# Optimization experiments

Measured on AMD Instinct MI355X. Metric: run time of the kernel, lower is better.

## Reference

```python
import jax, jax.numpy as jnp
import numpy as np

B, SQ, SK, D, DV = 16, 2048, 2048, 64, 64
DROPOUT_P = 0.1


def setup_inputs() -> dict:
    key = jax.random.key(0)
    k1, k2, k3, k4 = jax.random.split(key, 4)
    return {
        "query": jax.random.normal(k1, (B, SQ, D), dtype=jnp.float32),
        "key": jax.random.normal(k2, (B, SK, D), dtype=jnp.float32),
        "value": jax.random.normal(k3, (B, SK, DV), dtype=jnp.float32),
        "drop_mask": jax.random.uniform(k4, (B, SQ, SK), dtype=jnp.float32),
    }


def reference(query, key, value, drop_mask):
    # scaled dot-product attention with explicit score matrix, as in the module
    scale = jnp.sqrt(jnp.asarray(key.shape[-1], dtype=query.dtype))
    qk = jnp.einsum("bqd,bkd->bqk", query, key) / scale  # [B, SQ, SK]
    attn = jax.nn.softmax(qk, axis=-1)
    # dropout: keep where uniform > p, rescale by 1/(1-p)
    keep = (drop_mask > DROPOUT_P).astype(attn.dtype)
    attn = attn * keep / (1.0 - DROPOUT_P)
    return jnp.einsum("bqk,bkv->bqv", attn, value)  # [B, SQ, DV]
```

## Files before the change

### kernel.cpp

```cpp
#include <hip/hip_runtime.h>
#include <hip/hip_bf16.h>

#define B_ 16
#define SQ_ 2048
#define SK_ 2048
#define D_ 64
#define DV_ 64
#define INV_KEEP 1.1111111f

typedef float f4 __attribute__((ext_vector_type(4)));
typedef __bf16 bf16x2 __attribute__((ext_vector_type(2)));
typedef __bf16 bf16x8 __attribute__((ext_vector_type(8)));
typedef short s16x4 __attribute__((ext_vector_type(4)));
typedef unsigned int u32;
typedef unsigned int u32x2 __attribute__((ext_vector_type(2)));
typedef unsigned int u32x4 __attribute__((ext_vector_type(4)));

static __device__ __forceinline__ unsigned short bf16u(float f) {
    u32 u = __builtin_bit_cast(u32, f);
    u += 0x7fffu + ((u >> 16) & 1u);
    return (unsigned short)(u >> 16);
}
static __device__ __forceinline__ u32 pk2(float lo, float hi) {
    return (u32)bf16u(lo) | ((u32)bf16u(hi) << 16);
}
static __device__ __forceinline__ u32 pkc(float lo, float hi) {
    bf16x2 t = {(__bf16)lo, (__bf16)hi};
    return __builtin_bit_cast(u32, t);
}

static __device__ __forceinline__ void gload16(const void* g, void* l) {
    __builtin_amdgcn_global_load_lds(
        (const __attribute__((address_space(1))) unsigned int*)g,
        (__attribute__((address_space(3))) unsigned int*)l, 16, 0, 0);
}

static __device__ __forceinline__ f4 mfma16(s16x4 a, s16x4 b, f4 c) {
#if __has_builtin(__builtin_amdgcn_mfma_f32_16x16x16bf16_1k)
    return __builtin_amdgcn_mfma_f32_16x16x16bf16_1k(a, b, c, 0, 0, 0);
#else
    f4 d;
    asm("v_mfma_f32_16x16x16_bf16 %0, %1, %2, %3" : "=v"(d) : "v"(a), "v"(b), "v"(c));
    return d;
#endif
}

__global__ __launch_bounds__(256) void k_retile(const float* __restrict__ K,
                                                unsigned short* __restrict__ KbT) {
    int b = blockIdx.x >> 6, kt = blockIdx.x & 63;
    int t = threadIdx.x;
    int row = t >> 3, dc = t & 7;
    const float* src = K + ((size_t)(b * SK_ + kt * 32 + row)) * D_ + dc * 8;
    f4 a = *(const f4*)src;
    f4 b2 = *(const f4*)(src + 4);
    u32x4 w;
    w[0] = pk2(a.x, a.y); w[1] = pk2(a.z, a.w);
    w[2] = pk2(b2.x, b2.y); w[3] = pk2(b2.z, b2.w);
    *(u32x4*)(KbT + ((size_t)(b * 64 + kt)) * 2048 + (dc * 32 + row) * 8) = w;
}

__global__ __launch_bounds__(256) void v_retile(const float* __restrict__ V,
                                                unsigned short* __restrict__ VtT) {
    __shared__ float vt[32][65];
    int b = blockIdx.x >> 6, kt = blockIdx.x & 63;
    int t = threadIdx.x;
#pragma unroll
    for (int e = 0; e < 2; ++e) {
        int f = t * 2 + e;
        int row = f >> 4, c4 = (f & 15) * 4;
        *(f4*)&vt[row][c4] = *(const f4*)(V + ((size_t)(b * SK_ + kt * 32 + row)) * DV_ + c4);
    }
    __syncthreads();
    unsigned short* dst = VtT + ((size_t)(b * 64 + kt)) * 2048 + (size_t)t * 8;
    u32x4 w;
#pragma unroll
    for (int e = 0; e < 2; ++e) {
        int s = t * 2 + e;
        int kq = s >> 6, v = s & 63;
        w[e * 2 + 0] = pk2(vt[kq * 4 + 0][v], vt[kq * 4 + 1][v]);
        w[e * 2 + 1] = pk2(vt[kq * 4 + 2][v], vt[kq * 4 + 3][v]);
    }
    *(u32x4*)dst = w;
}

__global__ __launch_bounds__(256) void compress_mask(const float* __restrict__ mask,
                                                     u32* __restrict__ bits) {
    int strip = blockIdx.x;
    int b  = strip >> 7;
    int q0 = (strip & 127) << 4;
    int w    = threadIdx.x >> 6;
    int lane = threadIdx.x & 63;
    int g = lane >> 4, c = lane & 15;
    const float* mrow = mask + ((size_t)(b * SQ_ + q0 + c)) * SK_ + 4 * g;
    u32x4 outw;
#pragma unroll
    for (int tgl = 0; tgl < 4; ++tgl) {
        int tg = w * 4 + tgl;
        u32 word = 0;
#pragma unroll
        for (int ti = 0; ti < 4; ++ti) {
            const float* p = mrow + tg * 128 + ti * 32;
            f4 lo = *(const f4*)(p);
            f4 hi = *(const f4*)(p + 16);
            u32 by = 0;
#pragma unroll
            for (int r = 0; r < 4; ++r) {
                by |= (lo[r] > 0.1f ? (1u << r) : 0u);
                by |= (hi[r] > 0.1f ? (1u << (4 + r)) : 0u);
            }
            word |= by << (8 * ti);
        }
        outw[tgl] = word;
    }
    *(u32x4*)(bits + ((size_t)strip * 64 + lane) * 16 + w * 4) = outw;
}

template <int SPLIT>
__global__ __launch_bounds__(256) void attn_main(const float* __restrict__ Q,
                                                 const unsigned short* __restrict__ KbT,
                                                 const unsigned short* __restrict__ VtT,
                                                 const u32* __restrict__ bits,
                                                 float* __restrict__ out,
                                                 float* __restrict__ accP,
                                                 float* __restrict__ lP) {
    constexpr int NT32 = SK_ / SPLIT / 32;
    constexpr int NB = 512 * SPLIT;
    constexpr int NWORDS = NT32 / 4;
    __shared__ unsigned short sK[2][2048];
    __shared__ unsigned short sV[2][2048];

    int bswz = (blockIdx.x & 7) * (NB / 8) + (blockIdx.x >> 3);
    int wid  = threadIdx.x >> 6;
    int split = bswz & (SPLIT - 1);
    int strip = (bswz / SPLIT) * 4 + wid;
    int b  = strip >> 7;
    int q0 = (strip & 127) << 4;
    int lane = threadIdx.x & 63;
    int g = lane >> 4, c = lane & 15;

    const size_t tile0 = ((size_t)b * 64 + split * NT32) * 2048;
    const unsigned short* ksrc = KbT + tile0 + (size_t)threadIdx.x * 8;
    const unsigned short* vsrc = VtT + tile0 + (size_t)threadIdx.x * 8;

    gload16(ksrc, &sK[0][wid * 512]);
    gload16(vsrc, &sV[0][wid * 512]);

    u32 bwAll[NWORDS];
    {
        const u32* bbase = bits + ((size_t)strip * 64 + lane) * 16 + split * NWORDS;
#pragma unroll
        for (int n = 0; n < NWORDS / 4; ++n)
            *(u32x4*)&bwAll[n * 4] = *(const u32x4*)(bbase + n * 4);
    }

    bf16x8 qf[2];
    {
        const float* qp = Q + ((size_t)(b * SQ_ + q0 + c)) * D_ + 8 * g;
#pragma unroll
        for (int h = 0; h < 2; ++h) {
            f4 a  = *(const f4*)(qp + h * 32);
            f4 bq = *(const f4*)(qp + h * 32 + 4);
            u32x4 wq;
            wq[0] = pk2(a.x * 0.125f, a.y * 0.125f);
            wq[1] = pk2(a.z * 0.125f, a.w * 0.125f);
            wq[2] = pk2(bq.x * 0.125f, bq.y * 0.125f);
            wq[3] = pk2(bq.z * 0.125f, bq.w * 0.125f);
            qf[h] = __builtin_bit_cast(bf16x8, wq);
        }
    }

    const unsigned short* kbL = &sK[0][0] + g * 256 + c * 8;
    const unsigned short* vbL = &sV[0][0] + g * 256 + c * 4;

    f4 acc[4];
#pragma unroll
    for (int vb = 0; vb < 4; ++vb) acc[vb] = (f4){0.f, 0.f, 0.f, 0.f};
    float lsum[2][4];
#pragma unroll
    for (int t = 0; t < 2; ++t)
#pragma unroll
        for (int r = 0; r < 4; ++r) lsum[t][r] = 0.f;

#pragma unroll
    for (int kt = 0; kt < NT32; ++kt) {
        const int cur = kt & 1;
        if (kt + 1 < NT32) {
            gload16(ksrc + (size_t)(kt + 1) * 2048, &sK[cur ^ 1][wid * 512]);
            gload16(vsrc + (size_t)(kt + 1) * 2048, &sV[cur ^ 1][wid * 512]);
            asm volatile("s_waitcnt vmcnt(2)" ::: "memory");
        } else {
            asm volatile("s_waitcnt vmcnt(0)" ::: "memory");
        }
        __builtin_amdgcn_s_barrier();
        asm volatile("" ::: "memory");

        const unsigned short* kB = kbL + cur * 2048;
        const unsigned short* vB = vbL + cur * 2048;
        const u32 mby = (bwAll[kt >> 2] >> ((kt & 3) * 8)) & 0xFFu;

        f4 st[2];
#pragma unroll
        for (int t = 0; t < 2; ++t) {
            u32x4 k0 = *(const u32x4*)(kB + t * 128);
            u32x4 k1 = *(const u32x4*)(kB + 1024 + t * 128);
            st[t] = (f4){0.f, 0.f, 0.f, 0.f};
            st[t] = __builtin_amdgcn_mfma_f32_16x16x32_bf16(
                __builtin_bit_cast(bf16x8, k0), qf[0], st[t], 0, 0, 0);
            st[t] = __builtin_amdgcn_mfma_f32_16x16x32_bf16(
                __builtin_bit_cast(bf16x8, k1), qf[1], st[t], 0, 0, 0);
        }
        float pd[2][4];
#pragma unroll
        for (int t = 0; t < 2; ++t)
#pragma unroll
            for (int r = 0; r < 4; ++r) {
                float p = __expf(st[t][r]);
                lsum[t][r] += p;
                pd[t][r] = (mby & (1u << (4 * t + r))) ? p : 0.f;
            }
#pragma unroll
        for (int t = 0; t < 2; ++t) {
            u32x2 pw;
            pw[0] = pkc(pd[t][0], pd[t][1]);
            pw[1] = pkc(pd[t][2], pd[t][3]);
            s16x4 pb = __builtin_bit_cast(s16x4, pw);
#pragma unroll
            for (int vb = 0; vb < 4; ++vb) {
                u32x2 vv = *(const u32x2*)(vB + t * 1024 + vb * 64);
                acc[vb] = mfma16(__builtin_bit_cast(s16x4, vv), pb, acc[vb]);
            }
        }

        asm volatile("" ::: "memory");
        __builtin_amdgcn_s_barrier();
        asm volatile("" ::: "memory");
    }

    float lf = 0.f;
#pragma unroll
    for (int t = 0; t < 2; ++t)
#pragma unroll
        for (int r = 0; r < 4; ++r) lf += lsum[t][r];
    lf += __shfl_xor(lf, 16);
    lf += __shfl_xor(lf, 32);

    if constexpr (SPLIT == 1) {
        float li = INV_KEEP / lf;
        float* op = out + ((size_t)(b * SQ_ + q0 + c)) * DV_;
#pragma unroll
        for (int vb = 0; vb < 4; ++vb) {
            f4 o = acc[vb] * li;
            __builtin_nontemporal_store(o, (f4*)(op + 16 * vb + 4 * g));
        }
    } else {
        float* ap = accP + (((size_t)strip * SPLIT + split) * 64 + lane) * 16;
#pragma unroll
        for (int vb = 0; vb < 4; ++vb)
            *(f4*)(ap + 4 * vb) = acc[vb];
        if (g == 0)
            lP[((size_t)strip * SPLIT + split) * 16 + c] = lf;
    }
}

__global__ __launch_bounds__(256) void attn_combine(const float* __restrict__ accP,
                                                    const float* __restrict__ lP,
                                                    float* __restrict__ out) {
    __shared__ float sacc[4 * 1280];
    __shared__ float sl[64];
    int strip = blockIdx.x;
    int t = threadIdx.x;
    const float* src = accP + (size_t)strip * 4096;
#pragma unroll
    for (int s = 0; s < 4; ++s)
        *(f4*)&sacc[s * 1280 + (t >> 2) * 20 + (t & 3) * 4] = *(const f4*)(src + s * 1024 + t * 4);
    if (t < 64) sl[t] = lP[(size_t)strip * 64 + t];
    __syncthreads();

    int q = t >> 4, j = t & 15;
    float L = sl[q] + sl[16 + q] + sl[32 + q] + sl[48 + q];
    float inv = INV_KEEP / L;
    int base = (16 * (j & 3) + q) * 20 + 4 * (j >> 2);
    f4 o = (f4){0.f, 0.f, 0.f, 0.f};
#pragma unroll
    for (int s = 0; s < 4; ++s)
        o += *(const f4*)&sacc[s * 1280 + base];
    o *= inv;
    int b  = strip >> 7;
    int q0 = (strip & 127) << 4;
    __builtin_nontemporal_store(o, (f4*)(out + ((size_t)(b * SQ_ + q0 + q)) * DV_ + 4 * j));
}

extern "C" void kernel_launch(void* const* d_in, const int* in_sizes, int n_in,
                              void* d_out, int out_size, void* d_ws, size_t ws_size,
                              hipStream_t stream) {
    const float* Q = (const float*)d_in[0];
    const float* K = (const float*)d_in[1];
    const float* V = (const float*)d_in[2];
    const float* M = (const float*)d_in[3];
    float* out = (float*)d_out;

    char* ws = (char*)d_ws;
    unsigned short* KbT  = (unsigned short*)ws;
    unsigned short* VtT  = (unsigned short*)(ws + (size_t)4  * 1024 * 1024);
    u32*            bits = (u32*)           (ws + (size_t)8  * 1024 * 1024);
    float*          accP = (float*)         (ws + (size_t)16 * 1024 * 1024);
    float*          lP   = (float*)         (ws + (size_t)48 * 1024 * 1024);

    const size_t need_split = (size_t)48 * 1024 * 1024 + (size_t)2048 * 64 * 4;

    k_retile<<<1024, 256, 0, stream>>>(K, KbT);
    v_retile<<<1024, 256, 0, stream>>>(V, VtT);
    compress_mask<<<2048, 256, 0, stream>>>(M, bits);
    if (ws_size >= need_split) {
        attn_main<4><<<2048, 256, 0, stream>>>(Q, KbT, VtT, bits, out, accP, lP);
        attn_combine<<<2048, 256, 0, stream>>>(accP, lP, out);
    } else {
        attn_main<1><<<512, 256, 0, stream>>>(Q, KbT, VtT, bits, out, nullptr, nullptr);
    }
}
```

Measured before the change: 108.9 us.

## Fuse dropout mask read into attention kernel via LDS double-buffering

Removes the separate compress_mask kernel and instead streams the float dropout mask directly into shared memory alongside the K and V tiles in the main attention loop, thresholding it in place. This avoids one kernel launch and the write-then-read of the packed bit mask in workspace. In exchange, the main kernel adds 16 KB of LDS per block for a float mask double-buffer and issues more async loads per iteration, which may reduce occupancy and lengthen the memory wait in the pipelined loop.

```diff
diff --git a/kernel.cpp b/kernel.cpp
--- a/kernel.cpp
+++ b/kernel.cpp
@@ -83,51 +83,19 @@
     *(u32x4*)dst = w;
 }
 
-__global__ __launch_bounds__(256) void compress_mask(const float* __restrict__ mask,
-                                                     u32* __restrict__ bits) {
-    int strip = blockIdx.x;
-    int b  = strip >> 7;
-    int q0 = (strip & 127) << 4;
-    int w    = threadIdx.x >> 6;
-    int lane = threadIdx.x & 63;
-    int g = lane >> 4, c = lane & 15;
-    const float* mrow = mask + ((size_t)(b * SQ_ + q0 + c)) * SK_ + 4 * g;
-    u32x4 outw;
-#pragma unroll
-    for (int tgl = 0; tgl < 4; ++tgl) {
-        int tg = w * 4 + tgl;
-        u32 word = 0;
-#pragma unroll
-        for (int ti = 0; ti < 4; ++ti) {
-            const float* p = mrow + tg * 128 + ti * 32;
-            f4 lo = *(const f4*)(p);
-            f4 hi = *(const f4*)(p + 16);
-            u32 by = 0;
-#pragma unroll
-            for (int r = 0; r < 4; ++r) {
-                by |= (lo[r] > 0.1f ? (1u << r) : 0u);
-                by |= (hi[r] > 0.1f ? (1u << (4 + r)) : 0u);
-            }
-            word |= by << (8 * ti);
-        }
-        outw[tgl] = word;
-    }
-    *(u32x4*)(bits + ((size_t)strip * 64 + lane) * 16 + w * 4) = outw;
-}
-
 template <int SPLIT>
 __global__ __launch_bounds__(256) void attn_main(const float* __restrict__ Q,
                                                  const unsigned short* __restrict__ KbT,
                                                  const unsigned short* __restrict__ VtT,
-                                                 const u32* __restrict__ bits,
+                                                 const float* __restrict__ mask,
                                                  float* __restrict__ out,
                                                  float* __restrict__ accP,
                                                  float* __restrict__ lP) {
     constexpr int NT32 = SK_ / SPLIT / 32;
     constexpr int NB = 512 * SPLIT;
-    constexpr int NWORDS = NT32 / 4;
     __shared__ unsigned short sK[2][2048];
     __shared__ unsigned short sV[2][2048];
+    __shared__ float sM[2][2048];
 
     int bswz = (blockIdx.x & 7) * (NB / 8) + (blockIdx.x >> 3);
     int wid  = threadIdx.x >> 6;
@@ -135,23 +103,19 @@
     int strip = (bswz / SPLIT) * 4 + wid;
     int b  = strip >> 7;
     int q0 = (strip & 127) << 4;
+    int kb = split * (SK_ / SPLIT);
     int lane = threadIdx.x & 63;
     int g = lane >> 4, c = lane & 15;
 
     const size_t tile0 = ((size_t)b * 64 + split * NT32) * 2048;
     const unsigned short* ksrc = KbT + tile0 + (size_t)threadIdx.x * 8;
     const unsigned short* vsrc = VtT + tile0 + (size_t)threadIdx.x * 8;
+    const float* msrc = mask + ((size_t)(b * SQ_ + q0 + (lane & 15))) * SK_ + kb + (lane >> 4) * 4;
 
     gload16(ksrc, &sK[0][wid * 512]);
     gload16(vsrc, &sV[0][wid * 512]);
-
-    u32 bwAll[NWORDS];
-    {
-        const u32* bbase = bits + ((size_t)strip * 64 + lane) * 16 + split * NWORDS;
-#pragma unroll
-        for (int n = 0; n < NWORDS / 4; ++n)
-            *(u32x4*)&bwAll[n * 4] = *(const u32x4*)(bbase + n * 4);
-    }
+    gload16(msrc,      &sM[0][wid * 512]);
+    gload16(msrc + 16, &sM[0][wid * 512 + 256]);
 
     bf16x8 qf[2];
     {
@@ -171,6 +135,7 @@
 
     const unsigned short* kbL = &sK[0][0] + g * 256 + c * 8;
     const unsigned short* vbL = &sV[0][0] + g * 256 + c * 4;
+    const float* mbL = &sM[0][0] + wid * 512 + (g * 16 + c) * 4;
 
     f4 acc[4];
 #pragma unroll
@@ -187,7 +152,9 @@
         if (kt + 1 < NT32) {
             gload16(ksrc + (size_t)(kt + 1) * 2048, &sK[cur ^ 1][wid * 512]);
             gload16(vsrc + (size_t)(kt + 1) * 2048, &sV[cur ^ 1][wid * 512]);
-            asm volatile("s_waitcnt vmcnt(2)" ::: "memory");
+            gload16(msrc + (kt + 1) * 32,      &sM[cur ^ 1][wid * 512]);
+            gload16(msrc + (kt + 1) * 32 + 16, &sM[cur ^ 1][wid * 512 + 256]);
+            asm volatile("s_waitcnt vmcnt(4)" ::: "memory");
         } else {
             asm volatile("s_waitcnt vmcnt(0)" ::: "memory");
         }
@@ -196,7 +163,9 @@
 
         const unsigned short* kB = kbL + cur * 2048;
         const unsigned short* vB = vbL + cur * 2048;
-        const u32 mby = (bwAll[kt >> 2] >> ((kt & 3) * 8)) & 0xFFu;
+        const float* mB = mbL + cur * 2048;
+        f4 mk0 = *(const f4*)(mB);
+        f4 mk1 = *(const f4*)(mB + 256);
 
         f4 st[2];
 #pragma unroll
@@ -211,13 +180,15 @@
         }
         float pd[2][4];
 #pragma unroll
-        for (int t = 0; t < 2; ++t)
+        for (int t = 0; t < 2; ++t) {
+            const f4 mk = t ? mk1 : mk0;
 #pragma unroll
             for (int r = 0; r < 4; ++r) {
                 float p = __expf(st[t][r]);
                 lsum[t][r] += p;
-                pd[t][r] = (mby & (1u << (4 * t + r))) ? p : 0.f;
+                pd[t][r] = (mk[r] > 0.1f) ? p : 0.f;
             }
+        }
 #pragma unroll
         for (int t = 0; t < 2; ++t) {
             u32x2 pw;
@@ -301,20 +272,18 @@
 
     char* ws = (char*)d_ws;
     unsigned short* KbT  = (unsigned short*)ws;
-    unsigned short* VtT  = (unsigned short*)(ws + (size_t)4  * 1024 * 1024);
-    u32*            bits = (u32*)           (ws + (size_t)8  * 1024 * 1024);
-    float*          accP = (float*)         (ws + (size_t)16 * 1024 * 1024);
-    float*          lP   = (float*)         (ws + (size_t)48 * 1024 * 1024);
-
-    const size_t need_split = (size_t)48 * 1024 * 1024 + (size_t)2048 * 64 * 4;
+    unsigned short* VtT  = (unsigned short*)(ws + (size_t)4 * 1024 * 1024);
+    float*          accP = (float*)         (ws + (size_t)8 * 1024 * 1024);
+    float*          lP   = (float*)         (ws + (size_t)40 * 1024 * 1024);
+
+    const size_t need_split = (size_t)40 * 1024 * 1024 + (size_t)2048 * 4 * 16 * 4;
 
     k_retile<<<1024, 256, 0, stream>>>(K, KbT);
     v_retile<<<1024, 256, 0, stream>>>(V, VtT);
-    compress_mask<<<2048, 256, 0, stream>>>(M, bits);
     if (ws_size >= need_split) {
-        attn_main<4><<<2048, 256, 0, stream>>>(Q, KbT, VtT, bits, out, accP, lP);
+        attn_main<4><<<2048, 256, 0, stream>>>(Q, KbT, VtT, M, out, accP, lP);
         attn_combine<<<2048, 256, 0, stream>>>(accP, lP, out);
     } else {
-        attn_main<1><<<512, 256, 0, stream>>>(Q, KbT, VtT, bits, out, nullptr, nullptr);
-    }
-}
+        attn_main<1><<<512, 256, 0, stream>>>(Q, KbT, VtT, M, out, nullptr, nullptr);
+    }
+}
```

New measurement: 98.19 us. -9.8%, faster.
